# Kernel tuning notes

Hardware: AMD Instinct MI355X
Metric: run time of the kernel (lower is better)

The kernel has to match this reference:

```python
import jax, jax.numpy as jnp
import numpy as np

NUM_HEADS = 8
OUT_DIM = 32


def setup_inputs() -> dict:
    key = jax.random.key(0)
    ks = jax.random.split(key, 9)
    N, E, IN = 50000, 800000, 256
    HD = NUM_HEADS * OUT_DIM
    s = 1.0 / np.sqrt(IN)
    return {
        "h": jax.random.normal(ks[0], (N, IN), jnp.float32),
        "Wq": jax.random.normal(ks[1], (HD, IN), jnp.float32) * s,
        "bq": jax.random.normal(ks[2], (HD,), jnp.float32) * 0.01,
        "Wk": jax.random.normal(ks[3], (HD, IN), jnp.float32) * s,
        "bk": jax.random.normal(ks[4], (HD,), jnp.float32) * 0.01,
        "Wv": jax.random.normal(ks[5], (HD, IN), jnp.float32) * s,
        "bv": jax.random.normal(ks[6], (HD,), jnp.float32) * 0.01,
        "src": jax.random.randint(ks[7], (E,), 0, N, jnp.int32),
        "dst": jax.random.randint(ks[8], (E,), 0, N, jnp.int32),
    }


def reference(h, Wq, bq, Wk, bk, Wv, bv, src, dst):
    N = h.shape[0]
    H, D = NUM_HEADS, OUT_DIM
    # node projections -> [N, H, D]
    Q = (h @ Wq.T + bq).reshape(N, H, D)
    K = (h @ Wk.T + bk).reshape(N, H, D)
    V = (h @ Wv.T + bv).reshape(N, H, D)
    scale = jnp.asarray(np.sqrt(D), h.dtype)
    # per-edge scores: dot(K[src], Q[dst]) over D -> [E, H]
    score = jnp.exp(jnp.clip((K[src] * Q[dst]).sum(-1) / scale, -5.0, 5.0))
    # segment-softmax denominator over destination nodes -> [N, H]
    z = jax.ops.segment_sum(score, dst, num_segments=N)
    alpha = score / z[dst]  # [E, H]; every edge's dst has z > 0
    # weighted aggregation: sum over in-edges of alpha * V[src] -> [N, H, D]
    wV = jax.ops.segment_sum(V[src] * alpha[:, :, None], dst, num_segments=N)
    return wV
```

## Files before the change

### kernel.cpp

```cpp
#include <hip/hip_runtime.h>
#include <hip/hip_bf16.h>


typedef __attribute__((ext_vector_type(8))) short short8;
typedef __attribute__((ext_vector_type(8))) unsigned short ushortx8;
typedef __attribute__((ext_vector_type(4))) unsigned short ushortx4;
typedef __attribute__((ext_vector_type(4))) float floatx4;
typedef __attribute__((ext_vector_type(4))) int intx4;

__device__ __forceinline__ void g2l16(const void* g, void* l) {
    __builtin_amdgcn_global_load_lds(
        (const __attribute__((address_space(1))) unsigned int*)g,
        (__attribute__((address_space(3))) unsigned int*)l, 16, 0, 0);
}

__device__ __forceinline__ float bf2f(unsigned short u) {
    union { unsigned int i; float f; } c; c.i = ((unsigned int)u) << 16; return c.f;
}
__device__ __forceinline__ unsigned short f2bf(float f) {
    __hip_bfloat16 b = __float2bfloat16(f);
    return *reinterpret_cast<unsigned short*>(&b);
}

__global__ __launch_bounds__(256) void cvt_bf16(const float* __restrict__ src,
                                                unsigned short* __restrict__ dst, int n4) {
    int i = blockIdx.x * 256 + threadIdx.x;
    if (i >= n4) return;
    floatx4 f = __builtin_nontemporal_load((const floatx4*)src + i);
    ushortx4 u;
    u.x = f2bf(f.x); u.y = f2bf(f.y); u.z = f2bf(f.z); u.w = f2bf(f.w);
    ((ushortx4*)dst)[i] = u;
}

__global__ __launch_bounds__(256) void cvt_w3(const float* __restrict__ Wq,
                                              const float* __restrict__ Wk,
                                              const float* __restrict__ Wv,
                                              unsigned short* __restrict__ Wb, int n4) {
    int mat = blockIdx.y;
    const float* src = (mat == 0) ? Wq : (mat == 1) ? Wk : Wv;
    int i = blockIdx.x * 256 + threadIdx.x;
    if (i >= n4) return;
    floatx4 f = __builtin_nontemporal_load((const floatx4*)src + i);
    ushortx4 u;
    u.x = f2bf(f.x); u.y = f2bf(f.y); u.z = f2bf(f.z); u.w = f2bf(f.w);
    ((ushortx4*)(Wb + (size_t)mat * 65536))[i] = u;
}

__global__ __launch_bounds__(256) void qkv_gemm_mfma(
    const unsigned short* __restrict__ hb, const unsigned short* __restrict__ Wb,
    const float* __restrict__ bq, const float* __restrict__ bk, const float* __restrict__ bv,
    unsigned short* __restrict__ Qb, unsigned short* __restrict__ KV, int N)
{
    __shared__ unsigned short Ast[2][128 * 32];
    __shared__ unsigned short Bst[2][128 * 32];

    const int tid = threadIdx.x;
    const int wave = tid >> 6;
    const int lane = tid & 63;
    const int m = lane & 15;
    const int q = lane >> 4;
    const int wr = wave >> 1, wc = wave & 1;

    const int mbase = blockIdx.x * 128;
    const int mat = blockIdx.y >> 1;
    const int colbase = (blockIdx.y & 1) * 128;
    const int wrow0 = blockIdx.y * 128;

    const float* bias = (mat == 0) ? bq : (mat == 1) ? bk : bv;

    floatx4 acc[4][4] = {};

    for (int kk = 0; kk < 256; kk += 64) {
#pragma unroll
        for (int c = 0; c < 2; c++) {
#pragma unroll
            for (int t = 0; t < 2; t++) {
                int f = t * 256 + tid;
                int row = f >> 2, kc = f & 3;
                int grow = mbase + row; if (grow > N - 1) grow = N - 1;
                g2l16(hb + (size_t)grow * 256 + kk + c * 32 + kc * 8,
                      Ast[c] + (size_t)(t * 256 + wave * 64) * 8);
            }
#pragma unroll
            for (int t = 0; t < 2; t++) {
                int f = t * 256 + tid;
                int row = f >> 2, kc = f & 3;
                g2l16(Wb + (size_t)(wrow0 + row) * 256 + kk + c * 32 + kc * 8,
                      Bst[c] + (size_t)(t * 256 + wave * 64) * 8);
            }
        }
        __syncthreads();

#pragma unroll
        for (int c = 0; c < 2; c++) {
            short8 a[4], b[4];
#pragma unroll
            for (int i = 0; i < 4; i++) {
                int r = wr * 64 + i * 16 + m;
                a[i] = *(const short8*)&Ast[c][r * 32 + q * 8];
            }
#pragma unroll
            for (int j = 0; j < 4; j++) {
                int cc = wc * 64 + j * 16 + m;
                b[j] = *(const short8*)&Bst[c][cc * 32 + q * 8];
            }
#pragma unroll
            for (int i = 0; i < 4; i++)
#pragma unroll
                for (int j = 0; j < 4; j++)
                    acc[i][j] = __builtin_amdgcn_mfma_f32_16x16x32_bf16(a[i], b[j], acc[i][j], 0, 0, 0);
        }
        __syncthreads();
    }

    float bvj[4];
#pragma unroll
    for (int j = 0; j < 4; j++) bvj[j] = bias[colbase + wc * 64 + j * 16 + m];

    const int col0 = colbase + wc * 64 + m;
#pragma unroll
    for (int i = 0; i < 4; i++) {
#pragma unroll
        for (int r = 0; r < 4; r++) {
            int grow = mbase + wr * 64 + i * 16 + q * 4 + r;
            if (grow < N) {
                if (mat == 0) {
                    unsigned short* op = Qb + (size_t)grow * 256 + col0;
#pragma unroll
                    for (int j = 0; j < 4; j++)
                        __builtin_nontemporal_store(f2bf(acc[i][j][r] + bvj[j]), op + j * 16);
                } else {
                    unsigned short* op = KV + (size_t)grow * 512 + ((mat == 2) ? 256 : 0) + col0;
#pragma unroll
                    for (int j = 0; j < 4; j++)
                        op[j * 16] = f2bf(acc[i][j][r] + bvj[j]);
                }
            }
        }
    }
}

__global__ void count_deg(const int* __restrict__ dst, int* __restrict__ deg, int E) {
    int e4 = (blockIdx.x * 256 + threadIdx.x) * 4;
    if (e4 + 3 < E) {
        intx4 d = __builtin_nontemporal_load((const intx4*)(dst + e4));
        atomicAdd(&deg[d.x], 1); atomicAdd(&deg[d.y], 1);
        atomicAdd(&deg[d.z], 1); atomicAdd(&deg[d.w], 1);
    } else {
        for (int e = e4; e < E; e++) atomicAdd(&deg[dst[e]], 1);
    }
}

#define SCAN_CHUNK 2048

__global__ void scan_phase1(const int* __restrict__ deg, int* __restrict__ partials, int N) {
    __shared__ int sdata[256];
    int base = blockIdx.x * SCAN_CHUNK;
    int sum = 0;
#pragma unroll
    for (int i = 0; i < 8; i++) {
        int idx = base + threadIdx.x + i * 256;
        if (idx < N) sum += deg[idx];
    }
    sdata[threadIdx.x] = sum;
    __syncthreads();
    for (int s = 128; s > 0; s >>= 1) {
        if (threadIdx.x < (unsigned)s) sdata[threadIdx.x] += sdata[threadIdx.x + s];
        __syncthreads();
    }
    if (threadIdx.x == 0) partials[blockIdx.x] = sdata[0];
}

__global__ void scan_phase2(int* __restrict__ partials, int nb) {
    if (threadIdx.x == 0 && blockIdx.x == 0) {
        int run = 0;
        for (int i = 0; i < nb; i++) { int v = partials[i]; partials[i] = run; run += v; }
    }
}

__global__ void scan_phase3(const int* __restrict__ deg, const int* __restrict__ partials,
                            int* __restrict__ offsets, int* __restrict__ cursor, int N, int E) {
    __shared__ int sdata[256];
    int base = blockIdx.x * SCAN_CHUNK;
    int vals[8];
    int sum = 0;
#pragma unroll
    for (int i = 0; i < 8; i++) {
        int idx = base + threadIdx.x * 8 + i;
        vals[i] = (idx < N) ? deg[idx] : 0;
        sum += vals[i];
    }
    sdata[threadIdx.x] = sum;
    __syncthreads();
    for (int s = 1; s < 256; s <<= 1) {
        int v = sdata[threadIdx.x];
        int add = (threadIdx.x >= (unsigned)s) ? sdata[threadIdx.x - s] : 0;
        __syncthreads();
        sdata[threadIdx.x] = v + add;
        __syncthreads();
    }
    int excl = (threadIdx.x == 0) ? 0 : sdata[threadIdx.x - 1];
    int run = partials[blockIdx.x] + excl;
#pragma unroll
    for (int i = 0; i < 8; i++) {
        int idx = base + threadIdx.x * 8 + i;
        if (idx < N) { offsets[idx] = run; cursor[idx] = run; }
        run += vals[i];
    }
    if (blockIdx.x == 0 && threadIdx.x == 0) offsets[N] = E;
}

__global__ void scatter_edges(const int* __restrict__ dst, const int* __restrict__ src,
                              int* __restrict__ cursor, unsigned short* __restrict__ ssorted,
                              int E) {
    int e4 = (blockIdx.x * 256 + threadIdx.x) * 4;
    if (e4 + 3 < E) {
        intx4 d = __builtin_nontemporal_load((const intx4*)(dst + e4));
        intx4 s = __builtin_nontemporal_load((const intx4*)(src + e4));
        ssorted[atomicAdd(&cursor[d.x], 1)] = (unsigned short)s.x;
        ssorted[atomicAdd(&cursor[d.y], 1)] = (unsigned short)s.y;
        ssorted[atomicAdd(&cursor[d.z], 1)] = (unsigned short)s.z;
        ssorted[atomicAdd(&cursor[d.w], 1)] = (unsigned short)s.w;
    } else {
        for (int e = e4; e < E; e++)
            ssorted[atomicAdd(&cursor[dst[e]], 1)] = (unsigned short)src[e];
    }
}

__global__ __launch_bounds__(256) void edge_agg(
    const unsigned short* __restrict__ Qb, const unsigned short* __restrict__ KV,
    const int* __restrict__ offsets, const unsigned short* __restrict__ ssorted,
    float* __restrict__ out, int N)
{
    const int wave = threadIdx.x >> 6;
    const int lane = threadIdx.x & 63;
    const int half = lane >> 5;
    const int hl = lane & 31;
    const int n = blockIdx.x * 4 + wave;
    if (n >= N) return;

    float q[8];
    {
        ushortx8 qu = __builtin_nontemporal_load((const ushortx8*)(Qb + (size_t)n * 256 + hl * 8));
#pragma unroll
        for (int j = 0; j < 8; j++) q[j] = bf2f(qu[j]);
    }

    float acc[8] = {};
    float z = 0.f;
    const int beg = offsets[n], end = offsets[n + 1];
    const int len = end - beg;
    const int mid = beg + ((len + 1) >> 1);
    const float scale = 0.17677669529663687f;

    int i = half ? mid : beg;
    const int i1 = half ? end : mid;

    for (; i + 1 < i1; i += 2) {
        int s0 = __builtin_nontemporal_load(ssorted + i);
        int s1 = __builtin_nontemporal_load(ssorted + i + 1);
        const unsigned short* p0 = KV + (size_t)s0 * 512 + hl * 8;
        const unsigned short* p1 = KV + (size_t)s1 * 512 + hl * 8;
        ushortx8 k0 = *(const ushortx8*)p0;        ushortx8 v0 = *(const ushortx8*)(p0 + 256);
        ushortx8 k1 = *(const ushortx8*)p1;        ushortx8 v1 = *(const ushortx8*)(p1 + 256);

        float d0 = 0.f, d1 = 0.f;
#pragma unroll
        for (int j = 0; j < 8; j++) {
            d0 = fmaf(bf2f(k0[j]), q[j], d0);
            d1 = fmaf(bf2f(k1[j]), q[j], d1);
        }
        d0 += __shfl_xor(d0, 1); d0 += __shfl_xor(d0, 2);
        d1 += __shfl_xor(d1, 1); d1 += __shfl_xor(d1, 2);
        float e0 = __expf(fminf(5.f, fmaxf(-5.f, d0 * scale)));
        float e1 = __expf(fminf(5.f, fmaxf(-5.f, d1 * scale)));
        z += e0 + e1;
#pragma unroll
        for (int j = 0; j < 8; j++) {
            acc[j] = fmaf(e0, bf2f(v0[j]), acc[j]);
            acc[j] = fmaf(e1, bf2f(v1[j]), acc[j]);
        }
    }
    for (; i < i1; i++) {
        int s = __builtin_nontemporal_load(ssorted + i);
        const unsigned short* p = KV + (size_t)s * 512 + hl * 8;
        ushortx8 k8 = *(const ushortx8*)p;
        ushortx8 v8 = *(const ushortx8*)(p + 256);
        float d = 0.f;
#pragma unroll
        for (int j = 0; j < 8; j++) d = fmaf(bf2f(k8[j]), q[j], d);
        d += __shfl_xor(d, 1); d += __shfl_xor(d, 2);
        float sc = __expf(fminf(5.f, fmaxf(-5.f, d * scale)));
        z += sc;
#pragma unroll
        for (int j = 0; j < 8; j++) acc[j] = fmaf(sc, bf2f(v8[j]), acc[j]);
    }

    z += __shfl_xor(z, 32);
#pragma unroll
    for (int j = 0; j < 8; j++) acc[j] += __shfl_xor(acc[j], 32);

    if (half == 0) {
        float inv = (z > 0.f) ? 1.f / z : 0.f;
        floatx4 o0, o1;
        o0[0] = acc[0] * inv; o0[1] = acc[1] * inv; o0[2] = acc[2] * inv; o0[3] = acc[3] * inv;
        o1[0] = acc[4] * inv; o1[1] = acc[5] * inv; o1[2] = acc[6] * inv; o1[3] = acc[7] * inv;
        floatx4* op = (floatx4*)(out + (size_t)n * 256 + hl * 8);
        __builtin_nontemporal_store(o0, op);
        __builtin_nontemporal_store(o1, op + 1);
    }
}

extern "C" void kernel_launch(void* const* d_in, const int* in_sizes, int n_in,
                              void* d_out, int out_size, void* d_ws, size_t ws_size,
                              hipStream_t stream) {
    const float* h  = (const float*)d_in[0];
    const float* Wq = (const float*)d_in[1];
    const float* bq = (const float*)d_in[2];
    const float* Wk = (const float*)d_in[3];
    const float* bk = (const float*)d_in[4];
    const float* Wv = (const float*)d_in[5];
    const float* bv = (const float*)d_in[6];
    const int*   src = (const int*)d_in[7];
    const int*   dst = (const int*)d_in[8];
    float* out = (float*)d_out;

    const int N = in_sizes[0] / 256;
    const int E = in_sizes[7];

    size_t off = 0;
    auto alloc = [&](size_t bytes) {
        void* p = (char*)d_ws + off;
        off += (bytes + 255) & ~(size_t)255;
        return p;
    };
    unsigned short* Qb = (unsigned short*)alloc((size_t)N * 256 * 2);
    unsigned short* KV = (unsigned short*)alloc((size_t)N * 512 * 2);
    unsigned short* hb = (unsigned short*)alloc((size_t)N * 256 * 2);
    unsigned short* Wb = (unsigned short*)alloc((size_t)768 * 256 * 2);
    int* deg      = (int*)alloc((size_t)N * 4);
    int* offsets  = (int*)alloc((size_t)(N + 1) * 4);
    int* cursor   = (int*)alloc((size_t)N * 4);
    int* partials = (int*)alloc(1024 * 4);
    unsigned short* ssorted = (unsigned short*)alloc((size_t)E * 2);

    int n4h = (N * 256) / 4;
    cvt_bf16<<<(n4h + 255) / 256, 256, 0, stream>>>(h, hb, n4h);
    int n4w = (256 * 256) / 4;
    dim3 wgrid((n4w + 255) / 256, 3);
    cvt_w3<<<wgrid, 256, 0, stream>>>(Wq, Wk, Wv, Wb, n4w);

    dim3 ggrid((N + 127) / 128, 6);
    qkv_gemm_mfma<<<ggrid, 256, 0, stream>>>(hb, Wb, bq, bk, bv, Qb, KV, N);

    hipMemsetAsync(deg, 0, (size_t)N * 4, stream);
    int eblocks4 = (E + 1023) / 1024;
    count_deg<<<eblocks4, 256, 0, stream>>>(dst, deg, E);

    int nscan = (N + SCAN_CHUNK - 1) / SCAN_CHUNK;
    scan_phase1<<<nscan, 256, 0, stream>>>(deg, partials, N);
    scan_phase2<<<1, 64, 0, stream>>>(partials, nscan);
    scan_phase3<<<nscan, 256, 0, stream>>>(deg, partials, offsets, cursor, N, E);

    scatter_edges<<<eblocks4, 256, 0, stream>>>(dst, src, cursor, ssorted, E);

    int ablocks = (N + 3) / 4;
    edge_agg<<<ablocks, 256, 0, stream>>>(Qb, KV, offsets, ssorted, out, N);
}
```

Before: 366.7 us.

## Fuse prep kernels, pipeline GEMM K-loop with XCD remap, split edge aggregation

Merges the h/W bf16 conversions and degree counting into one launch to cut launch overhead. The QKV GEMM gets an XCD-aware 1D block remap and a double-buffered 32-wide K pipeline that uses explicit vmcnt waits and barriers, so global loads overlap with MFMA. The edge aggregation is split into four sequential launches over node ranges. The four-way split adds launches and may hurt rather than help.

Result: slower. 383.5 us (+4.6%).

```diff
diff --git a/kernel.cpp b/kernel.cpp
--- a/kernel.cpp
+++ b/kernel.cpp
@@ -22,28 +22,45 @@
     return *reinterpret_cast<unsigned short*>(&b);
 }
 
-__global__ __launch_bounds__(256) void cvt_bf16(const float* __restrict__ src,
-                                                unsigned short* __restrict__ dst, int n4) {
-    int i = blockIdx.x * 256 + threadIdx.x;
-    if (i >= n4) return;
-    floatx4 f = __builtin_nontemporal_load((const floatx4*)src + i);
-    ushortx4 u;
-    u.x = f2bf(f.x); u.y = f2bf(f.y); u.z = f2bf(f.z); u.w = f2bf(f.w);
-    ((ushortx4*)dst)[i] = u;
-}
-
-__global__ __launch_bounds__(256) void cvt_w3(const float* __restrict__ Wq,
-                                              const float* __restrict__ Wk,
-                                              const float* __restrict__ Wv,
-                                              unsigned short* __restrict__ Wb, int n4) {
-    int mat = blockIdx.y;
-    const float* src = (mat == 0) ? Wq : (mat == 1) ? Wk : Wv;
-    int i = blockIdx.x * 256 + threadIdx.x;
-    if (i >= n4) return;
-    floatx4 f = __builtin_nontemporal_load((const floatx4*)src + i);
-    ushortx4 u;
-    u.x = f2bf(f.x); u.y = f2bf(f.y); u.z = f2bf(f.z); u.w = f2bf(f.w);
-    ((ushortx4*)(Wb + (size_t)mat * 65536))[i] = u;
+__global__ __launch_bounds__(256) void prep(
+    const float* __restrict__ h, unsigned short* __restrict__ hb,
+    const float* __restrict__ Wq, const float* __restrict__ Wk, const float* __restrict__ Wv,
+    unsigned short* __restrict__ Wb,
+    const int* __restrict__ dst, int* __restrict__ deg,
+    int n4h, int n4w, int E, int bh, int bw)
+{
+    const int bid = blockIdx.x;
+    const int tid = threadIdx.x;
+    if (bid < bh) {
+        int i = bid * 256 + tid;
+        if (i < n4h) {
+            floatx4 f = __builtin_nontemporal_load((const floatx4*)h + i);
+            ushortx4 u;
+            u.x = f2bf(f.x); u.y = f2bf(f.y); u.z = f2bf(f.z); u.w = f2bf(f.w);
+            ((ushortx4*)hb)[i] = u;
+        }
+    } else if (bid < bh + 3 * bw) {
+        int b2 = bid - bh;
+        int mat = b2 / bw;
+        const float* src = (mat == 0) ? Wq : (mat == 1) ? Wk : Wv;
+        int i = (b2 % bw) * 256 + tid;
+        if (i < n4w) {
+            floatx4 f = __builtin_nontemporal_load((const floatx4*)src + i);
+            ushortx4 u;
+            u.x = f2bf(f.x); u.y = f2bf(f.y); u.z = f2bf(f.z); u.w = f2bf(f.w);
+            ((ushortx4*)(Wb + (size_t)mat * 65536))[i] = u;
+        }
+    } else {
+        int b3 = bid - bh - 3 * bw;
+        int e4 = (b3 * 256 + tid) * 4;
+        if (e4 + 3 < E) {
+            intx4 d = __builtin_nontemporal_load((const intx4*)(dst + e4));
+            atomicAdd(&deg[d.x], 1); atomicAdd(&deg[d.y], 1);
+            atomicAdd(&deg[d.z], 1); atomicAdd(&deg[d.w], 1);
+        } else {
+            for (int e = e4; e < E; e++) atomicAdd(&deg[dst[e]], 1);
+        }
+    }
 }
 
 __global__ __launch_bounds__(256) void qkv_gemm_mfma(
@@ -61,56 +78,74 @@
     const int q = lane >> 4;
     const int wr = wave >> 1, wc = wave & 1;
 
-    const int mbase = blockIdx.x * 128;
-    const int mat = blockIdx.y >> 1;
-    const int colbase = (blockIdx.y & 1) * 128;
-    const int wrow0 = blockIdx.y * 128;
+    const int nwg = gridDim.x;
+    const int orig = blockIdx.x;
+    const int q8 = nwg >> 3, r8 = nwg & 7;
+    const int xcd = orig & 7;
+    const int wgid = (xcd < r8 ? xcd * (q8 + 1) : r8 * (q8 + 1) + (xcd - r8) * q8)
+                     + (orig >> 3);
+    const int bx = wgid / 6;
+    const int by = wgid % 6;
+
+    const int mbase = bx * 128;
+    const int mat = by >> 1;
+    const int colbase = (by & 1) * 128;
+    const int wrow0 = by * 128;
 
     const float* bias = (mat == 0) ? bq : (mat == 1) ? bk : bv;
 
     floatx4 acc[4][4] = {};
 
-    for (int kk = 0; kk < 256; kk += 64) {
-#pragma unroll
-        for (int c = 0; c < 2; c++) {
-#pragma unroll
-            for (int t = 0; t < 2; t++) {
-                int f = t * 256 + tid;
-                int row = f >> 2, kc = f & 3;
-                int grow = mbase + row; if (grow > N - 1) grow = N - 1;
-                g2l16(hb + (size_t)grow * 256 + kk + c * 32 + kc * 8,
-                      Ast[c] + (size_t)(t * 256 + wave * 64) * 8);
-            }
-#pragma unroll
-            for (int t = 0; t < 2; t++) {
-                int f = t * 256 + tid;
-                int row = f >> 2, kc = f & 3;
-                g2l16(Wb + (size_t)(wrow0 + row) * 256 + kk + c * 32 + kc * 8,
-                      Bst[c] + (size_t)(t * 256 + wave * 64) * 8);
-            }
-        }
-        __syncthreads();
-
-#pragma unroll
-        for (int c = 0; c < 2; c++) {
-            short8 a[4], b[4];
-#pragma unroll
-            for (int i = 0; i < 4; i++) {
-                int r = wr * 64 + i * 16 + m;
-                a[i] = *(const short8*)&Ast[c][r * 32 + q * 8];
-            }
-#pragma unroll
-            for (int j = 0; j < 4; j++) {
-                int cc = wc * 64 + j * 16 + m;
-                b[j] = *(const short8*)&Bst[c][cc * 32 + q * 8];
-            }
-#pragma unroll
-            for (int i = 0; i < 4; i++)
-#pragma unroll
-                for (int j = 0; j < 4; j++)
-                    acc[i][j] = __builtin_amdgcn_mfma_f32_16x16x32_bf16(a[i], b[j], acc[i][j], 0, 0, 0);
-        }
-        __syncthreads();
+    auto stage = [&](int g) {
+        int buf = g & 1;
+        int koff = g * 32;
+#pragma unroll
+        for (int t = 0; t < 2; t++) {
+            int f = t * 256 + tid;
+            int row = f >> 2, kc = f & 3;
+            int grow = mbase + row; if (grow > N - 1) grow = N - 1;
+            g2l16(hb + (size_t)grow * 256 + koff + kc * 8,
+                  Ast[buf] + (size_t)(t * 256 + wave * 64) * 8);
+        }
+#pragma unroll
+        for (int t = 0; t < 2; t++) {
+            int f = t * 256 + tid;
+            int row = f >> 2, kc = f & 3;
+            g2l16(Wb + (size_t)(wrow0 + row) * 256 + koff + kc * 8,
+                  Bst[buf] + (size_t)(t * 256 + wave * 64) * 8);
+        }
+    };
+
+    stage(0);
+    stage(1);
+
+#pragma unroll
+    for (int g = 0; g < 8; g++) {
+        const int buf = g & 1;
+        asm volatile("s_waitcnt vmcnt(4)" ::: "memory");
+        __builtin_amdgcn_s_barrier();
+        __builtin_amdgcn_sched_barrier(0);
+
+        short8 a[4], b[4];
+#pragma unroll
+        for (int i = 0; i < 4; i++) {
+            int r = wr * 64 + i * 16 + m;
+            a[i] = *(const short8*)&Ast[buf][r * 32 + q * 8];
+        }
+#pragma unroll
+        for (int j = 0; j < 4; j++) {
+            int cc = wc * 64 + j * 16 + m;
+            b[j] = *(const short8*)&Bst[buf][cc * 32 + q * 8];
+        }
+#pragma unroll
+        for (int i = 0; i < 4; i++)
+#pragma unroll
+            for (int j = 0; j < 4; j++)
+                acc[i][j] = __builtin_amdgcn_mfma_f32_16x16x32_bf16(a[i], b[j], acc[i][j], 0, 0, 0);
+
+        __builtin_amdgcn_s_barrier();
+        __builtin_amdgcn_sched_barrier(0);
+        if (g < 6) stage(g + 2);
     }
 
     float bvj[4];
@@ -137,17 +172,6 @@
                 }
             }
         }
-    }
-}
-
-__global__ void count_deg(const int* __restrict__ dst, int* __restrict__ deg, int E) {
-    int e4 = (blockIdx.x * 256 + threadIdx.x) * 4;
-    if (e4 + 3 < E) {
-        intx4 d = __builtin_nontemporal_load((const intx4*)(dst + e4));
-        atomicAdd(&deg[d.x], 1); atomicAdd(&deg[d.y], 1);
-        atomicAdd(&deg[d.z], 1); atomicAdd(&deg[d.w], 1);
-    } else {
-        for (int e = e4; e < E; e++) atomicAdd(&deg[dst[e]], 1);
     }
 }
 
@@ -230,14 +254,14 @@
 __global__ __launch_bounds__(256) void edge_agg(
     const unsigned short* __restrict__ Qb, const unsigned short* __restrict__ KV,
     const int* __restrict__ offsets, const unsigned short* __restrict__ ssorted,
-    float* __restrict__ out, int N)
+    float* __restrict__ out, int n0, int n1)
 {
     const int wave = threadIdx.x >> 6;
     const int lane = threadIdx.x & 63;
     const int half = lane >> 5;
     const int hl = lane & 31;
-    const int n = blockIdx.x * 4 + wave;
-    if (n >= N) return;
+    const int n = n0 + blockIdx.x * 4 + wave;
+    if (n >= n1) return;
 
     float q[8];
     {
@@ -344,26 +368,29 @@
     int* partials = (int*)alloc(1024 * 4);
     unsigned short* ssorted = (unsigned short*)alloc((size_t)E * 2);
 
+    hipMemsetAsync(deg, 0, (size_t)N * 4, stream);
     int n4h = (N * 256) / 4;
-    cvt_bf16<<<(n4h + 255) / 256, 256, 0, stream>>>(h, hb, n4h);
     int n4w = (256 * 256) / 4;
-    dim3 wgrid((n4w + 255) / 256, 3);
-    cvt_w3<<<wgrid, 256, 0, stream>>>(Wq, Wk, Wv, Wb, n4w);
-
-    dim3 ggrid((N + 127) / 128, 6);
-    qkv_gemm_mfma<<<ggrid, 256, 0, stream>>>(hb, Wb, bq, bk, bv, Qb, KV, N);
-
-    hipMemsetAsync(deg, 0, (size_t)N * 4, stream);
-    int eblocks4 = (E + 1023) / 1024;
-    count_deg<<<eblocks4, 256, 0, stream>>>(dst, deg, E);
+    int bh = (n4h + 255) / 256;
+    int bw = (n4w + 255) / 256;
+    int bc = (E + 1023) / 1024;
+    prep<<<bh + 3 * bw + bc, 256, 0, stream>>>(h, hb, Wq, Wk, Wv, Wb, dst, deg,
+                                               n4h, n4w, E, bh, bw);
+
+    int nb6 = ((N + 127) / 128) * 6;
+    qkv_gemm_mfma<<<nb6, 256, 0, stream>>>(hb, Wb, bq, bk, bv, Qb, KV, N);
 
     int nscan = (N + SCAN_CHUNK - 1) / SCAN_CHUNK;
     scan_phase1<<<nscan, 256, 0, stream>>>(deg, partials, N);
     scan_phase2<<<1, 64, 0, stream>>>(partials, nscan);
     scan_phase3<<<nscan, 256, 0, stream>>>(deg, partials, offsets, cursor, N, E);
-
-    scatter_edges<<<eblocks4, 256, 0, stream>>>(dst, src, cursor, ssorted, E);
-
-    int ablocks = (N + 3) / 4;
-    edge_agg<<<ablocks, 256, 0, stream>>>(Qb, KV, offsets, ssorted, out, N);
-}
+    scatter_edges<<<bc, 256, 0, stream>>>(dst, src, cursor, ssorted, E);
+
+    int q4 = (N + 3) / 4;
+    for (int c = 0; c < 4; c++) {
+        int lo = c * q4;
+        if (lo >= N) break;
+        int cnt = (N - lo < q4) ? (N - lo) : q4;
+        edge_agg<<<(cnt + 3) / 4, 256, 0, stream>>>(Qb, KV, offsets, ssorted, out, lo, lo + cnt);
+    }
+}
```
